# Kernel tuning notes

Hardware: AMD Instinct MI355X
Metric: run time of the kernel (lower is better)

Reference implementation:

```python
import jax, jax.numpy as jnp
import numpy as np

DIM = 1024
CTX_DIM = 768
HEADS = 16
D_HEAD = 64
INNER = HEADS * D_HEAD  # 1024
EPS = 1e-5


def _layernorm(x, g, b):
    mu = jnp.mean(x, axis=-1, keepdims=True)
    var = jnp.mean(jnp.square(x - mu), axis=-1, keepdims=True)
    return (x - mu) * jax.lax.rsqrt(var + EPS) * g + b


def setup_inputs() -> dict:
    key = jax.random.key(0)
    ks = jax.random.split(key, 8)
    s = lambda fan_in: 1.0 / np.sqrt(fan_in)
    return {
        "x": jax.random.normal(ks[0], (4, 2048, DIM), dtype=jnp.float32),
        "context": jax.random.normal(ks[1], (4, 2048, CTX_DIM), dtype=jnp.float32),
        "norm_g": jnp.ones((DIM,), jnp.float32),
        "norm_b": jnp.zeros((DIM,), jnp.float32),
        "normc_g": jnp.ones((CTX_DIM,), jnp.float32),
        "normc_b": jnp.zeros((CTX_DIM,), jnp.float32),
        # Linear weights stored [in, out] so y = x @ W (bias=False as in module)
        "Wq": jax.random.uniform(ks[2], (DIM, INNER), jnp.float32, -s(DIM), s(DIM)),
        "Wk": jax.random.uniform(ks[3], (CTX_DIM, INNER), jnp.float32, -s(CTX_DIM), s(CTX_DIM)),
        "Wv": jax.random.uniform(ks[4], (CTX_DIM, INNER), jnp.float32, -s(CTX_DIM), s(CTX_DIM)),
        "Wo": jax.random.uniform(ks[5], (INNER, DIM), jnp.float32, -s(INNER), s(INNER)),
    }


def reference(x, context, norm_g, norm_b, normc_g, normc_b, Wq, Wk, Wv, Wo):
    b, n, _ = x.shape
    m = context.shape[1]
    xn = _layernorm(x, norm_g, norm_b)
    cn = _layernorm(context, normc_g, normc_b)
    # project and split heads: b n (h d) -> b h n d
    split = lambda t, L: t.reshape(b, L, HEADS, D_HEAD).transpose(0, 2, 1, 3)
    q = split(xn @ Wq, n)
    k = split(cn @ Wk, m)
    v = split(cn @ Wv, m)
    sim = jnp.einsum('bhid,bhjd->bhij', q, k) / np.sqrt(D_HEAD)
    attn = jax.nn.softmax(sim, axis=-1)  # dropout p=0 (eval): identity
    out = jnp.einsum('bhij,bhjd->bhid', attn, v)
    out = out.transpose(0, 2, 1, 3).reshape(b, n, INNER)
    return out @ Wo
```

## Files before the change

kernel.cpp:

```cpp
#include <hip/hip_runtime.h>
#include <hip/hip_bf16.h>
#include <stdint.h>

#define TOK 8192
#define NQ 2048
#define DIMX 1024
#define CTXD 768

typedef __attribute__((ext_vector_type(8))) short short8;
typedef __attribute__((ext_vector_type(4))) float f32x4;
typedef __attribute__((ext_vector_type(2))) unsigned int u32x2;

typedef __attribute__((address_space(3))) uint32_t lds_u32_t;
typedef const __attribute__((address_space(1))) uint32_t glb_u32_t;

__device__ __forceinline__ void gld_lds16(const void* g, void* l) {
  __builtin_amdgcn_global_load_lds((glb_u32_t*)g, (lds_u32_t*)l, 16, 0, 0);
}

__device__ __forceinline__ uint16_t f2bf(float f) {
  union { float f; uint32_t u; } v; v.f = f;
  uint32_t r = v.u + 0x7fffu + ((v.u >> 16) & 1u);
  return (uint16_t)(r >> 16);
}

__device__ __forceinline__ uint32_t cvt_pk_bf16(float lo, float hi) {
  uint32_t d;
  asm("v_cvt_pk_bf16_f32 %0, %1, %2" : "=v"(d) : "v"(lo), "v"(hi));
  return d;
}

__device__ __forceinline__ float fexp2(float x) {
#if __has_builtin(__builtin_amdgcn_exp2f)
  return __builtin_amdgcn_exp2f(x);
#else
  float d;
  asm volatile("v_exp_f32 %0, %1\n\ts_nop 1" : "=v"(d) : "v"(x));
  return d;
#endif
}

template<int COLS, int NW>
__global__ __launch_bounds__(COLS/4)
void ln_cast_kernel(const float* __restrict__ x, const float* __restrict__ g,
                    const float* __restrict__ b, uint16_t* __restrict__ out) {
  int row = blockIdx.x;
  int tid = threadIdx.x;
  const float* xr = x + (size_t)row * COLS + tid * 4;
  float4 v = *(const float4*)xr;
  float s1 = v.x + v.y + v.z + v.w;
  float s2 = v.x*v.x + v.y*v.y + v.z*v.z + v.w*v.w;
#pragma unroll
  for (int off = 1; off < 64; off <<= 1) {
    s1 += __shfl_xor(s1, off);
    s2 += __shfl_xor(s2, off);
  }
  __shared__ float sm[2][NW];
  int w = tid >> 6;
  if ((tid & 63) == 0) { sm[0][w] = s1; sm[1][w] = s2; }
  __syncthreads();
  float t1 = 0.f, t2 = 0.f;
#pragma unroll
  for (int i = 0; i < NW; i++) { t1 += sm[0][i]; t2 += sm[1][i]; }
  float mu = t1 * (1.0f / COLS);
  float var = t2 * (1.0f / COLS) - mu * mu;
  float rs = rsqrtf(var + 1e-5f);
  float4 gv = *(const float4*)(g + tid * 4);
  float4 bv = *(const float4*)(b + tid * 4);
  uint32_t lo = (uint32_t)f2bf((v.x - mu) * rs * gv.x + bv.x) |
                ((uint32_t)f2bf((v.y - mu) * rs * gv.y + bv.y) << 16);
  uint32_t hi = (uint32_t)f2bf((v.z - mu) * rs * gv.z + bv.z) |
                ((uint32_t)f2bf((v.w - mu) * rs * gv.w + bv.w) << 16);
  uint2 o; o.x = lo; o.y = hi;
  *(uint2*)(out + (size_t)row * COLS + tid * 4) = o;
}

__global__ __launch_bounds__(256)
void transpose_cast4_kernel(const float* __restrict__ W0, const float* __restrict__ W1,
                            const float* __restrict__ W2, const float* __restrict__ W3,
                            uint16_t* __restrict__ T0, uint16_t* __restrict__ T1,
                            uint16_t* __restrict__ T2, uint16_t* __restrict__ T3) {
  int z = blockIdx.z;
  const float* W = (z == 0) ? W0 : (z == 1) ? W1 : (z == 2) ? W2 : W3;
  uint16_t* WT   = (z == 0) ? T0 : (z == 1) ? T1 : (z == 2) ? T2 : T3;
  int K = (z == 1 || z == 2) ? CTXD : DIMX;
  const int N = DIMX;
  int c0 = blockIdx.x * 32, r0 = blockIdx.y * 32;
  if (r0 >= K) return;
  __shared__ float t[32][33];
  int tx = threadIdx.x & 31, ty = threadIdx.x >> 5;
#pragma unroll
  for (int i = 0; i < 4; i++)
    t[ty + 8*i][tx] = W[(size_t)(r0 + ty + 8*i) * N + c0 + tx];
  __syncthreads();
#pragma unroll
  for (int i = 0; i < 4; i++)
    WT[(size_t)(c0 + ty + 8*i) * K + r0 + tx] = f2bf(t[tx][ty + 8*i]);
}

template<int OUT_BF16, int PERMC>
__global__ __launch_bounds__(256)
void gemm_bt_kernel(const uint16_t* __restrict__ A, const uint16_t* __restrict__ BT,
                    void* __restrict__ C, int M, int N, int K, float oscale) {
  __shared__ __align__(16) uint16_t Al[128 * 64];
  __shared__ __align__(16) uint16_t Bl[128 * 64];
  int tid = threadIdx.x;
  int l = tid & 63, w = tid >> 6;
  int g = l >> 4, r = l & 15;
  int wm = w >> 1, wn = w & 1;
  int flat = blockIdx.y * gridDim.x + blockIdx.x;
  int nwg = gridDim.x * gridDim.y;
  flat = (flat & 7) * (nwg >> 3) + (flat >> 3);
  int bx = flat & (gridDim.x - 1);
  int by = flat / gridDim.x;
  int n0 = bx * 128, m0 = by * 128;
  f32x4 acc[4][4] = {};
  int srow = tid >> 3, sslot = tid & 7;

  for (int kt = 0; kt < K; kt += 64) {
    __syncthreads();
#pragma unroll
    for (int c = 0; c < 4; c++) {
      int row = c * 32 + srow;
      int ksrc = (sslot * 8) ^ ((row & 7) << 3);
      gld_lds16(A + (size_t)(m0 + row) * K + kt + ksrc, Al + (c * 256 + w * 64) * 8);
    }
#pragma unroll
    for (int c = 0; c < 4; c++) {
      int row = c * 32 + srow;
      int ksrc = (sslot * 8) ^ ((row & 7) << 3);
      gld_lds16(BT + (size_t)(n0 + row) * K + kt + ksrc, Bl + (c * 256 + w * 64) * 8);
    }
    __syncthreads();
#pragma unroll
    for (int kk = 0; kk < 2; kk++) {
      int kb2 = (kk * 32 + g * 8) * 2;
      short8 af[4], bfr[4];
#pragma unroll
      for (int mf = 0; mf < 4; mf++) {
        int row = wm * 64 + mf * 16 + r;
        af[mf] = *(const short8*)((const char*)Al + row * 128 + (kb2 ^ ((row & 7) << 4)));
      }
#pragma unroll
      for (int nf = 0; nf < 4; nf++) {
        int row = wn * 64 + nf * 16 + r;
        bfr[nf] = *(const short8*)((const char*)Bl + row * 128 + (kb2 ^ ((row & 7) << 4)));
      }
#pragma unroll
      for (int mf = 0; mf < 4; mf++)
#pragma unroll
        for (int nf = 0; nf < 4; nf++)
          acc[mf][nf] = __builtin_amdgcn_mfma_f32_16x16x32_bf16(af[mf], bfr[nf], acc[mf][nf], 0, 0, 0);
    }
  }
#pragma unroll
  for (int mf = 0; mf < 4; mf++) {
#pragma unroll
    for (int i = 0; i < 4; i++) {
      size_t row = (size_t)m0 + wm * 64 + mf * 16 + g * 4 + i;
      if (PERMC) {
        u32x2 pk;
        pk.x = cvt_pk_bf16(acc[mf][0][i], acc[mf][1][i]);
        pk.y = cvt_pk_bf16(acc[mf][2][i], acc[mf][3][i]);
        *(u32x2*)((uint16_t*)C + row * N + n0 + wn * 64 + r * 4) = pk;
      } else {
#pragma unroll
        for (int nf = 0; nf < 4; nf++) {
          int col = n0 + wn * 64 + nf * 16 + r;
          float val = acc[mf][nf][i] * oscale;
          if (OUT_BF16) ((uint16_t*)C)[row * N + col] = f2bf(val);
          else          ((float*)C)[row * N + col] = val;
        }
      }
    }
  }
}

__global__ __launch_bounds__(256)
void attn_kernel(const uint16_t* __restrict__ Q, const uint16_t* __restrict__ Kp,
                 const uint16_t* __restrict__ VT, uint16_t* __restrict__ O) {
  __shared__ __align__(16) uint16_t Kl[64 * 64];
  __shared__ __align__(16) uint16_t Vl[64 * 64];
  __shared__ __align__(16) uint16_t Pl[4 * 32 * 64];
  int tid = threadIdx.x;
  int l = tid & 63, w = tid >> 6;
  int g = l >> 4, r = l & 15;
  int flat = blockIdx.y * 16 + blockIdx.x;
  flat = (flat & 7) * 128 + (flat >> 3);
  int q0 = (flat & 15) * 128;
  int bh = flat >> 4, b = bh >> 4, h = bh & 15;

  short8 qa[2][2];
#pragma unroll
  for (int qb = 0; qb < 2; qb++) {
    const uint16_t* qptr = Q + (size_t)(b * NQ + q0 + w * 32 + qb * 16 + r) * DIMX + h * 64;
    qa[qb][0] = *(const short8*)(qptr + g * 8);
    qa[qb][1] = *(const short8*)(qptr + 32 + g * 8);
  }

  float lpart[2][4] = {};
  f32x4 oacc[2][4] = {};

  const uint16_t* kbase = Kp + (size_t)(b * NQ) * DIMX + h * 64;
  const uint16_t* vbase = VT + (size_t)(h * 64) * TOK + b * NQ;
  int srow = tid >> 3, sslot = tid & 7;

  char* pwb = (char*)Pl + w * 4096;
  const char* prb = (const char*)Pl + w * 4096;

  for (int kv0 = 0; kv0 < NQ; kv0 += 64) {
    __syncthreads();
#pragma unroll
    for (int c = 0; c < 2; c++) {
      int key = c * 32 + srow;
      int dsrc = (sslot * 8) ^ ((key & 7) << 3);
      gld_lds16(kbase + (size_t)(kv0 + key) * DIMX + dsrc, Kl + (c * 256 + w * 64) * 8);
    }
#pragma unroll
    for (int c = 0; c < 2; c++) {
      int d = c * 32 + srow;
      int ksrc = (sslot * 8) ^ ((d & 7) << 3);
      gld_lds16(vbase + (size_t)d * TOK + kv0 + ksrc, Vl + (c * 256 + w * 64) * 8);
    }
    __syncthreads();

    f32x4 sc[2][4] = {};
#pragma unroll
    for (int kk = 0; kk < 2; kk++) {
      int kb2 = (kk * 32 + g * 8) * 2;
#pragma unroll
      for (int c = 0; c < 4; c++) {
        int row = c * 16 + r;
        short8 kf = *(const short8*)((const char*)Kl + row * 128 + (kb2 ^ ((row & 7) << 4)));
        sc[0][c] = __builtin_amdgcn_mfma_f32_16x16x32_bf16(qa[0][kk], kf, sc[0][c], 0, 0, 0);
        sc[1][c] = __builtin_amdgcn_mfma_f32_16x16x32_bf16(qa[1][kk], kf, sc[1][c], 0, 0, 0);
      }
    }

#pragma unroll
    for (int qb = 0; qb < 2; qb++) {
#pragma unroll
      for (int i = 0; i < 4; i++) {
        float p0 = fexp2(sc[qb][0][i]);
        float p1 = fexp2(sc[qb][1][i]);
        float p2 = fexp2(sc[qb][2][i]);
        float p3 = fexp2(sc[qb][3][i]);
        lpart[qb][i] += (p0 + p1) + (p2 + p3);
        u32x2 pk;
        pk.x = cvt_pk_bf16(p0, p1);
        pk.y = cvt_pk_bf16(p2, p3);
        int q = qb * 16 + g * 4 + i;
        *(u32x2*)(pwb + q * 128 + ((r * 8) ^ ((q & 7) << 4))) = pk;
      }
    }

#pragma unroll
    for (int kk = 0; kk < 2; kk++) {
      int kb2 = (kk * 64 + g * 16);
      short8 pa0 = *(const short8*)(prb + (0 * 16 + r) * 128 + (kb2 ^ ((r & 7) << 4)));
      short8 pa1 = *(const short8*)(prb + (1 * 16 + r) * 128 + (kb2 ^ ((r & 7) << 4)));
#pragma unroll
      for (int c = 0; c < 4; c++) {
        int row = c * 16 + r;
        short8 vf = *(const short8*)((const char*)Vl + row * 128 + ((kk * 32 + g * 8) * 2 ^ ((row & 7) << 4)));
        oacc[0][c] = __builtin_amdgcn_mfma_f32_16x16x32_bf16(pa0, vf, oacc[0][c], 0, 0, 0);
        oacc[1][c] = __builtin_amdgcn_mfma_f32_16x16x32_bf16(pa1, vf, oacc[1][c], 0, 0, 0);
      }
    }
  }

#pragma unroll
  for (int qb = 0; qb < 2; qb++)
#pragma unroll
    for (int i = 0; i < 4; i++) {
      lpart[qb][i] += __shfl_xor(lpart[qb][i], 1);
      lpart[qb][i] += __shfl_xor(lpart[qb][i], 2);
      lpart[qb][i] += __shfl_xor(lpart[qb][i], 4);
      lpart[qb][i] += __shfl_xor(lpart[qb][i], 8);
    }

#pragma unroll
  for (int qb = 0; qb < 2; qb++) {
    uint16_t* obase = O + (size_t)(b * NQ + q0 + w * 32 + qb * 16) * DIMX + h * 64;
#pragma unroll
    for (int i = 0; i < 4; i++) {
      float inv = 1.f / lpart[qb][i];
#pragma unroll
      for (int c = 0; c < 4; c++)
        obase[(size_t)(g * 4 + i) * DIMX + c * 16 + r] = f2bf(oacc[qb][c][i] * inv);
    }
  }
}

extern "C" void kernel_launch(void* const* d_in, const int* in_sizes, int n_in,
                              void* d_out, int out_size, void* d_ws, size_t ws_size,
                              hipStream_t stream) {
  (void)in_sizes; (void)n_in; (void)out_size; (void)ws_size;
  const float* x       = (const float*)d_in[0];
  const float* ctx     = (const float*)d_in[1];
  const float* norm_g  = (const float*)d_in[2];
  const float* norm_b  = (const float*)d_in[3];
  const float* normc_g = (const float*)d_in[4];
  const float* normc_b = (const float*)d_in[5];
  const float* Wq      = (const float*)d_in[6];
  const float* Wk      = (const float*)d_in[7];
  const float* Wv      = (const float*)d_in[8];
  const float* Wo      = (const float*)d_in[9];

  char* p = (char*)d_ws;
  uint16_t* xn  = (uint16_t*)p; p += (size_t)TOK * DIMX * 2;
  uint16_t* cn  = (uint16_t*)p; p += (size_t)TOK * CTXD * 2;
  uint16_t* WqT = (uint16_t*)p; p += (size_t)DIMX * DIMX * 2;
  uint16_t* WkT = (uint16_t*)p; p += (size_t)DIMX * CTXD * 2;
  uint16_t* WvT = (uint16_t*)p; p += (size_t)DIMX * CTXD * 2;
  uint16_t* WoT = (uint16_t*)p; p += (size_t)DIMX * DIMX * 2;
  uint16_t* Qs  = (uint16_t*)p; p += (size_t)TOK * DIMX * 2;
  uint16_t* Ks  = (uint16_t*)p; p += (size_t)TOK * DIMX * 2;
  uint16_t* VTs = (uint16_t*)p; p += (size_t)DIMX * TOK * 2;
  uint16_t* AO  = (uint16_t*)p; p += (size_t)TOK * DIMX * 2;

  ln_cast_kernel<DIMX, 4><<<TOK, 256, 0, stream>>>(x, norm_g, norm_b, xn);
  ln_cast_kernel<CTXD, 3><<<TOK, 192, 0, stream>>>(ctx, normc_g, normc_b, cn);

  transpose_cast4_kernel<<<dim3(DIMX/32, DIMX/32, 4), 256, 0, stream>>>(
      Wq, Wk, Wv, Wo, WqT, WkT, WvT, WoT);

  const float qscale = 0.125f * 1.44269504088896340736f;
  gemm_bt_kernel<1,0><<<dim3(DIMX/128, TOK/128), 256, 0, stream>>>(xn, WqT, Qs, TOK, DIMX, DIMX, qscale);
  gemm_bt_kernel<1,0><<<dim3(DIMX/128, TOK/128), 256, 0, stream>>>(cn, WkT, Ks, TOK, DIMX, CTXD, 1.f);
  gemm_bt_kernel<1,1><<<dim3(TOK/128, DIMX/128), 256, 0, stream>>>(WvT, cn, VTs, DIMX, TOK, CTXD, 1.f);

  attn_kernel<<<dim3(NQ/128, 64), 256, 0, stream>>>(Qs, Ks, VTs, AO);

  gemm_bt_kernel<0,0><<<dim3(DIMX/128, TOK/128), 256, 0, stream>>>(AO, WoT, d_out, TOK, DIMX, DIMX, 1.f);
}
```

Baseline: 211.8 us.

## Merge Q/K/V projection GEMMs into one launch and raise MFMA wave priority

Replaces the three separate Q, K and V projection GEMM launches with a single 1536-block kernel. Each block picks its sub-problem from a remapped flat block index, which removes launch gaps and tail underutilisation between the GEMMs. The attention kernel also wraps its two MFMA phases in s_setprio(1)/s_setprio(0) so the scheduler favours waves issuing matrix ops over those doing exp and LDS work. The fused kernel now takes out_bf16 and permc as runtime flags instead of template parameters, which adds some branching and could cost registers. The (flat&7)*192 swizzle also mixes blocks from the three GEMMs in odd ways.

Result: faster. 206.4 us (-2.6%).

```diff
diff --git a/kernel.cpp b/kernel.cpp
--- a/kernel.cpp
+++ b/kernel.cpp
@@ -98,82 +98,115 @@
     WT[(size_t)(c0 + ty + 8*i) * K + r0 + tx] = f2bf(t[tx][ty + 8*i]);
 }
 
-template<int OUT_BF16, int PERMC>
-__global__ __launch_bounds__(256)
-void gemm_bt_kernel(const uint16_t* __restrict__ A, const uint16_t* __restrict__ BT,
-                    void* __restrict__ C, int M, int N, int K, float oscale) {
-  __shared__ __align__(16) uint16_t Al[128 * 64];
-  __shared__ __align__(16) uint16_t Bl[128 * 64];
-  int tid = threadIdx.x;
+__device__ __forceinline__ void gemm_block(
+    const uint16_t* __restrict__ A, const uint16_t* __restrict__ BT,
+    void* __restrict__ C, int N, int K, float oscale,
+    int out_bf16, int permc, int m0, int n0,
+    uint16_t* Al, uint16_t* Bl, int tid) {
   int l = tid & 63, w = tid >> 6;
   int g = l >> 4, r = l & 15;
   int wm = w >> 1, wn = w & 1;
+  f32x4 acc[4][4] = {};
+  int srow = tid >> 3, sslot = tid & 7;
+
+  for (int kt = 0; kt < K; kt += 64) {
+    __syncthreads();
+#pragma unroll
+    for (int c = 0; c < 4; c++) {
+      int row = c * 32 + srow;
+      int ksrc = (sslot * 8) ^ ((row & 7) << 3);
+      gld_lds16(A + (size_t)(m0 + row) * K + kt + ksrc, Al + (c * 256 + w * 64) * 8);
+    }
+#pragma unroll
+    for (int c = 0; c < 4; c++) {
+      int row = c * 32 + srow;
+      int ksrc = (sslot * 8) ^ ((row & 7) << 3);
+      gld_lds16(BT + (size_t)(n0 + row) * K + kt + ksrc, Bl + (c * 256 + w * 64) * 8);
+    }
+    __syncthreads();
+#pragma unroll
+    for (int kk = 0; kk < 2; kk++) {
+      int kb2 = (kk * 32 + g * 8) * 2;
+      short8 af[4], bfr[4];
+#pragma unroll
+      for (int mf = 0; mf < 4; mf++) {
+        int row = wm * 64 + mf * 16 + r;
+        af[mf] = *(const short8*)((const char*)Al + row * 128 + (kb2 ^ ((row & 7) << 4)));
+      }
+#pragma unroll
+      for (int nf = 0; nf < 4; nf++) {
+        int row = wn * 64 + nf * 16 + r;
+        bfr[nf] = *(const short8*)((const char*)Bl + row * 128 + (kb2 ^ ((row & 7) << 4)));
+      }
+#pragma unroll
+      for (int mf = 0; mf < 4; mf++)
+#pragma unroll
+        for (int nf = 0; nf < 4; nf++)
+          acc[mf][nf] = __builtin_amdgcn_mfma_f32_16x16x32_bf16(af[mf], bfr[nf], acc[mf][nf], 0, 0, 0);
+    }
+  }
+#pragma unroll
+  for (int mf = 0; mf < 4; mf++) {
+#pragma unroll
+    for (int i = 0; i < 4; i++) {
+      size_t row = (size_t)m0 + wm * 64 + mf * 16 + g * 4 + i;
+      if (permc) {
+        u32x2 pk;
+        pk.x = cvt_pk_bf16(acc[mf][0][i], acc[mf][1][i]);
+        pk.y = cvt_pk_bf16(acc[mf][2][i], acc[mf][3][i]);
+        *(u32x2*)((uint16_t*)C + row * N + n0 + wn * 64 + r * 4) = pk;
+      } else {
+#pragma unroll
+        for (int nf = 0; nf < 4; nf++) {
+          int col = n0 + wn * 64 + nf * 16 + r;
+          float val = acc[mf][nf][i] * oscale;
+          if (out_bf16) ((uint16_t*)C)[row * N + col] = f2bf(val);
+          else          ((float*)C)[row * N + col] = val;
+        }
+      }
+    }
+  }
+}
+
+__global__ __launch_bounds__(256)
+void gemm_proj3_kernel(const uint16_t* __restrict__ xn, const uint16_t* __restrict__ cn,
+                       const uint16_t* __restrict__ WqT, const uint16_t* __restrict__ WkT,
+                       const uint16_t* __restrict__ WvT,
+                       uint16_t* __restrict__ Qs, uint16_t* __restrict__ Ks,
+                       uint16_t* __restrict__ VTs, float qscale) {
+  __shared__ __align__(16) uint16_t Al[128 * 64];
+  __shared__ __align__(16) uint16_t Bl[128 * 64];
+  int flat = blockIdx.x;
+  flat = (flat & 7) * 192 + (flat >> 3);
+  const uint16_t* A; const uint16_t* BT; uint16_t* C;
+  int N, K, permc, m0, n0;
+  float osc = 1.f;
+  if (flat < 512) {
+    A = xn; BT = WqT; C = Qs; N = DIMX; K = DIMX; permc = 0; osc = qscale;
+    n0 = (flat & 7) * 128; m0 = (flat >> 3) * 128;
+  } else if (flat < 1024) {
+    int f = flat - 512;
+    A = cn; BT = WkT; C = Ks; N = DIMX; K = CTXD; permc = 0;
+    n0 = (f & 7) * 128; m0 = (f >> 3) * 128;
+  } else {
+    int f = flat - 1024;
+    A = WvT; BT = cn; C = VTs; N = TOK; K = CTXD; permc = 1;
+    n0 = (f & 63) * 128; m0 = (f >> 6) * 128;
+  }
+  gemm_block(A, BT, C, N, K, osc, 1, permc, m0, n0, Al, Bl, threadIdx.x);
+}
+
+__global__ __launch_bounds__(256)
+void gemm_out_kernel(const uint16_t* __restrict__ A, const uint16_t* __restrict__ BT,
+                     float* __restrict__ C, int M, int N, int K) {
+  __shared__ __align__(16) uint16_t Al[128 * 64];
+  __shared__ __align__(16) uint16_t Bl[128 * 64];
   int flat = blockIdx.y * gridDim.x + blockIdx.x;
   int nwg = gridDim.x * gridDim.y;
   flat = (flat & 7) * (nwg >> 3) + (flat >> 3);
   int bx = flat & (gridDim.x - 1);
   int by = flat / gridDim.x;
-  int n0 = bx * 128, m0 = by * 128;
-  f32x4 acc[4][4] = {};
-  int srow = tid >> 3, sslot = tid & 7;
-
-  for (int kt = 0; kt < K; kt += 64) {
-    __syncthreads();
-#pragma unroll
-    for (int c = 0; c < 4; c++) {
-      int row = c * 32 + srow;
-      int ksrc = (sslot * 8) ^ ((row & 7) << 3);
-      gld_lds16(A + (size_t)(m0 + row) * K + kt + ksrc, Al + (c * 256 + w * 64) * 8);
-    }
-#pragma unroll
-    for (int c = 0; c < 4; c++) {
-      int row = c * 32 + srow;
-      int ksrc = (sslot * 8) ^ ((row & 7) << 3);
-      gld_lds16(BT + (size_t)(n0 + row) * K + kt + ksrc, Bl + (c * 256 + w * 64) * 8);
-    }
-    __syncthreads();
-#pragma unroll
-    for (int kk = 0; kk < 2; kk++) {
-      int kb2 = (kk * 32 + g * 8) * 2;
-      short8 af[4], bfr[4];
-#pragma unroll
-      for (int mf = 0; mf < 4; mf++) {
-        int row = wm * 64 + mf * 16 + r;
-        af[mf] = *(const short8*)((const char*)Al + row * 128 + (kb2 ^ ((row & 7) << 4)));
-      }
-#pragma unroll
-      for (int nf = 0; nf < 4; nf++) {
-        int row = wn * 64 + nf * 16 + r;
-        bfr[nf] = *(const short8*)((const char*)Bl + row * 128 + (kb2 ^ ((row & 7) << 4)));
-      }
-#pragma unroll
-      for (int mf = 0; mf < 4; mf++)
-#pragma unroll
-        for (int nf = 0; nf < 4; nf++)
-          acc[mf][nf] = __builtin_amdgcn_mfma_f32_16x16x32_bf16(af[mf], bfr[nf], acc[mf][nf], 0, 0, 0);
-    }
-  }
-#pragma unroll
-  for (int mf = 0; mf < 4; mf++) {
-#pragma unroll
-    for (int i = 0; i < 4; i++) {
-      size_t row = (size_t)m0 + wm * 64 + mf * 16 + g * 4 + i;
-      if (PERMC) {
-        u32x2 pk;
-        pk.x = cvt_pk_bf16(acc[mf][0][i], acc[mf][1][i]);
-        pk.y = cvt_pk_bf16(acc[mf][2][i], acc[mf][3][i]);
-        *(u32x2*)((uint16_t*)C + row * N + n0 + wn * 64 + r * 4) = pk;
-      } else {
-#pragma unroll
-        for (int nf = 0; nf < 4; nf++) {
-          int col = n0 + wn * 64 + nf * 16 + r;
-          float val = acc[mf][nf][i] * oscale;
-          if (OUT_BF16) ((uint16_t*)C)[row * N + col] = f2bf(val);
-          else          ((float*)C)[row * N + col] = val;
-        }
-      }
-    }
-  }
+  gemm_block(A, BT, C, N, K, 1.f, 0, 0, by * 128, bx * 128, Al, Bl, threadIdx.x);
 }
 
 __global__ __launch_bounds__(256)
@@ -225,6 +258,7 @@
     __syncthreads();
 
     f32x4 sc[2][4] = {};
+    __builtin_amdgcn_s_setprio(1);
 #pragma unroll
     for (int kk = 0; kk < 2; kk++) {
       int kb2 = (kk * 32 + g * 8) * 2;
@@ -236,6 +270,7 @@
         sc[1][c] = __builtin_amdgcn_mfma_f32_16x16x32_bf16(qa[1][kk], kf, sc[1][c], 0, 0, 0);
       }
     }
+    __builtin_amdgcn_s_setprio(0);
 
 #pragma unroll
     for (int qb = 0; qb < 2; qb++) {
@@ -254,6 +289,7 @@
       }
     }
 
+    __builtin_amdgcn_s_setprio(1);
 #pragma unroll
     for (int kk = 0; kk < 2; kk++) {
       int kb2 = (kk * 64 + g * 16);
@@ -267,6 +303,7 @@
         oacc[1][c] = __builtin_amdgcn_mfma_f32_16x16x32_bf16(pa1, vf, oacc[1][c], 0, 0, 0);
       }
     }
+    __builtin_amdgcn_s_setprio(0);
   }
 
 #pragma unroll
@@ -326,11 +363,9 @@
       Wq, Wk, Wv, Wo, WqT, WkT, WvT, WoT);
 
   const float qscale = 0.125f * 1.44269504088896340736f;
-  gemm_bt_kernel<1,0><<<dim3(DIMX/128, TOK/128), 256, 0, stream>>>(xn, WqT, Qs, TOK, DIMX, DIMX, qscale);
-  gemm_bt_kernel<1,0><<<dim3(DIMX/128, TOK/128), 256, 0, stream>>>(cn, WkT, Ks, TOK, DIMX, CTXD, 1.f);
-  gemm_bt_kernel<1,1><<<dim3(TOK/128, DIMX/128), 256, 0, stream>>>(WvT, cn, VTs, DIMX, TOK, CTXD, 1.f);
+  gemm_proj3_kernel<<<1536, 256, 0, stream>>>(xn, cn, WqT, WkT, WvT, Qs, Ks, VTs, qscale);
 
   attn_kernel<<<dim3(NQ/128, 64), 256, 0, stream>>>(Qs, Ks, VTs, AO);
 
-  gemm_bt_kernel<0,0><<<dim3(DIMX/128, TOK/128), 256, 0, stream>>>(AO, WoT, d_out, TOK, DIMX, DIMX, 1.f);
-}
+  gemm_out_kernel<<<dim3(DIMX/128, TOK/128), 256, 0, stream>>>(AO, WoT, (float*)d_out, TOK, DIMX, DIMX);
+}
```
